# Kernel optimization log

Measured on AMD Instinct MI355X. Metric: run time of the kernel, lower is better.

Reference implementation:

```python
import jax, jax.numpy as jnp
import numpy as np

TEMPERATURE = 2.0


def _offdiag_idx(n):
    # flat indices of the off-diagonal entries of an [n, n] matrix, row-major,
    # reshaped to [n, n-1] (matches torch masked_select(~eye).view(n, n-1))
    idx = np.arange(n * n).reshape(n, n)
    return jnp.asarray(idx[~np.eye(n, dtype=bool)].reshape(n, n - 1))


def setup_inputs() -> dict:
    key = jax.random.key(0)
    k1, k2, k3, k4 = jax.random.split(key, 4)
    B, D = 256, 512
    return {
        "wt_emb": jax.random.normal(k1, (B, D), dtype=jnp.float32),
        "mt_emb": jax.random.normal(k2, (B, D), dtype=jnp.float32),
        "label_wt": jax.random.uniform(k3, (B,), dtype=jnp.float32),
        "label_mt": jax.random.uniform(k4, (B,), dtype=jnp.float32),
    }


def reference(wt_emb, mt_emb, label_wt, label_mt):
    t = TEMPERATURE
    features = jnp.concatenate([wt_emb, mt_emb], axis=0)            # [n, D]
    labels = jnp.concatenate([label_wt, label_mt], axis=0)[:, None]  # [n, 1]
    n = features.shape[0]

    # L1 label differences: [n, n]
    label_diffs = jnp.abs(labels[:, None, :] - labels[None, :, :]).sum(-1)

    # negative L2 feature distances (safe sqrt: diagonal is exactly 0)
    diff = features[:, None, :] - features[None, :, :]               # [n, n, D]
    sq = jnp.sum(diff * diff, axis=-1)                               # [n, n]
    dist = jnp.where(sq > 0, jnp.sqrt(jnp.where(sq > 0, sq, 1.0)), 0.0)
    logits = -dist / t
    logits = logits - jax.lax.stop_gradient(jnp.max(logits, axis=1, keepdims=True))
    exp_logits = jnp.exp(logits)

    # drop diagonal -> [n, n-1]
    off = _offdiag_idx(n)
    lo = logits.reshape(-1)[off]
    eo = exp_logits.reshape(-1)[off]
    ldo = label_diffs.reshape(-1)[off]

    # vectorized over positive index k: mask[i, k, j] = ld[i, j] >= ld[i, k]
    neg_mask = ldo[:, None, :] >= ldo[:, :, None]                    # [n, n-1, n-1]
    denom = jnp.sum(jnp.where(neg_mask, eo[:, None, :], 0.0), axis=-1)  # [n, n-1]
    pos_log_probs = lo - jnp.log(denom)                              # [n, n-1]
    return -jnp.sum(pos_log_probs) / (n * (n - 1))
```

## Files before the change

### kernel.cpp

```cpp
#include <hip/hip_runtime.h>

#define N 512
#define B 256
#define D 512
#define NT 512
#define NBLK (N / 2)

#define WS_SL    0
#define WS_RANK  N
#define WS_NORM  (2 * N)
#define WS_PART  (3 * N)

__global__ __launch_bounds__(NT) void rank_norm_kernel(
    const float* __restrict__ wt, const float* __restrict__ mt,
    const float* __restrict__ lwt, const float* __restrict__ lmt,
    float* __restrict__ ws)
{
    const int t = threadIdx.x, b = blockIdx.x;
    __shared__ float slab[N];
    __shared__ int scnt[32];
    slab[t] = (t < B) ? lwt[t] : lmt[t - B];
    if (t < 32) scnt[t] = 0;
    __syncthreads();

    const int jj = t & 31, j = b * 32 + jj, c = t >> 5;
    const float lj = slab[j];
    int r = 0;
    #pragma unroll 8
    for (int x = c * 32; x < c * 32 + 32; ++x) {
        const float v = slab[x];
        r += (v < lj || (v == lj && x < j)) ? 1 : 0;
    }
    atomicAdd(&scnt[jj], r);

    const int row = b * 32 + (t >> 4), s16 = t & 15;
    const float* F = (row < B) ? (wt + (size_t)row * D) : (mt + (size_t)(row - B) * D);
    const float4* F4 = (const float4*)F;
    float nacc = 0.f;
    #pragma unroll
    for (int q = 0; q < 8; ++q) {
        const float4 v = F4[s16 + 16 * q];
        nacc += v.x * v.x + v.y * v.y + v.z * v.z + v.w * v.w;
    }
    nacc += __shfl_down(nacc, 8, 16);
    nacc += __shfl_down(nacc, 4, 16);
    nacc += __shfl_down(nacc, 2, 16);
    nacc += __shfl_down(nacc, 1, 16);
    if (s16 == 0) ws[WS_NORM + row] = nacc;

    __syncthreads();
    if (t < 32) {
        const int r2 = scnt[t], j2 = b * 32 + t;
        ws[WS_SL + r2] = slab[j2];
        ((int*)ws)[WS_RANK + j2] = r2;
    }
}

__global__ __launch_bounds__(NT) void rnc_main(
    const float* __restrict__ wt, const float* __restrict__ mt,
    const float* __restrict__ lwt, const float* __restrict__ lmt,
    float* __restrict__ ws)
{
    const int b = blockIdx.x, i0 = 2 * b, i1 = 2 * b + 1;
    const int t = threadIdx.x;
    const int w = t >> 6, lane = t & 63, g = lane >> 4, s = lane & 15;

    __shared__ float sl[N];
    __shared__ int   srk[N];
    __shared__ float snm[N];
    __shared__ __align__(16) float sp0[N];
    __shared__ __align__(16) float sf0[N];
    __shared__ __align__(16) float sp1[N];
    __shared__ __align__(16) float sf1[N];
    __shared__ float sred[NT / 64];

    sl[t]  = ws[WS_SL + t];
    srk[t] = ((const int*)ws)[WS_RANK + t];
    snm[t] = ws[WS_NORM + t];

    const float* Fi0 = (i0 < B) ? (wt + (size_t)i0 * D) : (mt + (size_t)(i0 - B) * D);
    const float* Fi1 = (i1 < B) ? (wt + (size_t)i1 * D) : (mt + (size_t)(i1 - B) * D);
    const float4* Fi04 = (const float4*)Fi0;
    const float4* Fi14 = (const float4*)Fi1;
    float4 fr0[8], fr1[8];
    #pragma unroll
    for (int q = 0; q < 8; ++q) { fr0[q] = Fi04[s + 16 * q]; fr1[q] = Fi14[s + 16 * q]; }
    const float li0 = (i0 < B) ? lwt[i0] : lmt[i0 - B];
    const float li1 = (i1 < B) ? lwt[i1] : lmt[i1 - B];
    __syncthreads();
    const float ni0 = snm[i0], ni1 = snm[i1];

    float lg_acc = 0.f;
    const int wg = w * 4 + g;
    for (int m = 0; m < 16; ++m) {
        const int j = wg + 32 * m;
        const float* Fj = (j < B) ? (wt + (size_t)j * D) : (mt + (size_t)(j - B) * D);
        const float4* Fj4 = (const float4*)Fj;
        float a0 = 0.f, a1 = 0.f;
        #pragma unroll
        for (int q = 0; q < 8; ++q) {
            const float4 v = Fj4[s + 16 * q];
            a0 += fr0[q].x * v.x + fr0[q].y * v.y + fr0[q].z * v.z + fr0[q].w * v.w;
            a1 += fr1[q].x * v.x + fr1[q].y * v.y + fr1[q].z * v.z + fr1[q].w * v.w;
        }
        a0 += __shfl_down(a0, 8, 16); a1 += __shfl_down(a1, 8, 16);
        a0 += __shfl_down(a0, 4, 16); a1 += __shfl_down(a1, 4, 16);
        a0 += __shfl_down(a0, 2, 16); a1 += __shfl_down(a1, 2, 16);
        a0 += __shfl_down(a0, 1, 16); a1 += __shfl_down(a1, 1, 16);
        if (s == 0) {
            const float nj = snm[j];
            const float d0 = fmaxf(ni0 + nj - 2.f * a0, 0.f);
            const float d1 = fmaxf(ni1 + nj - 2.f * a1, 0.f);
            const float lg0 = -0.5f * sqrtf(d0);
            const float lg1 = -0.5f * sqrtf(d1);
            lg_acc += lg0 + lg1;
            const int pos = srk[j];
            const float e0 = (j == i0) ? 0.f : __expf(lg0);
            const float e1 = (j == i1) ? 0.f : __expf(lg1);
            sp0[pos] = e0; sf0[pos] = e0;
            sp1[pos] = e1; sf1[pos] = e1;
        }
    }
    __syncthreads();

    if (w < 4) {
        float* arr = (w == 0) ? sp0 : (w == 1) ? sf0 : (w == 2) ? sp1 : sf1;
        float4* a4 = (float4*)arr;
        float4 u0 = a4[lane * 2], u1 = a4[lane * 2 + 1];
        float v0 = u0.x, v1 = u0.y, v2 = u0.z, v3 = u0.w;
        float v4 = u1.x, v5 = u1.y, v6 = u1.z, v7 = u1.w;
        if ((w & 1) == 0) {
            v1 += v0; v2 += v1; v3 += v2; v4 += v3; v5 += v4; v6 += v5; v7 += v6;
            float x = v7;
            #pragma unroll
            for (int off = 1; off < 64; off <<= 1) {
                const float y = __shfl_up(x, off, 64);
                if (lane >= off) x += y;
            }
            float ex = __shfl_up(x, 1, 64);
            if (lane == 0) ex = 0.f;
            v0 += ex; v1 += ex; v2 += ex; v3 += ex; v4 += ex; v5 += ex; v6 += ex; v7 += ex;
        } else {
            v6 += v7; v5 += v6; v4 += v5; v3 += v4; v2 += v3; v1 += v2; v0 += v1;
            float x = v0;
            #pragma unroll
            for (int off = 1; off < 64; off <<= 1) {
                const float y = __shfl_down(x, off, 64);
                if (lane + off < 64) x += y;
            }
            float ex = __shfl_down(x, 1, 64);
            if (lane == 63) ex = 0.f;
            v0 += ex; v1 += ex; v2 += ex; v3 += ex; v4 += ex; v5 += ex; v6 += ex; v7 += ex;
        }
        a4[lane * 2]     = make_float4(v0, v1, v2, v3);
        a4[lane * 2 + 1] = make_float4(v4, v5, v6, v7);
    }
    __syncthreads();

    const int ri0 = srk[i0], ri1 = srk[i1];
    float local = lg_acc;
    #pragma unroll
    for (int p = 0; p < 2; ++p) {
        const int idx = t + p * NT;
        const int row = idx >> 9;
        const int x = idx & (N - 1);
        const int ri = row ? ri1 : ri0;
        const float li = row ? li1 : li0;
        const float* SP = row ? sp1 : sp0;
        const float* SF = row ? sf1 : sf0;
        if (x != ri) {
            const float th = fabsf(li - sl[x]);
            int lo = 0, hi = ri + 1;
            while (lo < hi) {
                const int mid = (lo + hi) >> 1;
                if (fabsf(li - sl[mid]) >= th) lo = mid + 1; else hi = mid;
            }
            const int a = lo;
            lo = ri + 1; hi = N;
            while (lo < hi) {
                const int mid = (lo + hi) >> 1;
                if (fabsf(li - sl[mid]) >= th) hi = mid; else lo = mid + 1;
            }
            const int bb = lo;
            const float denom = ((a > 0) ? SP[a - 1] : 0.f) + ((bb < N) ? SF[bb] : 0.f);
            local -= __logf(denom);
        }
    }

    #pragma unroll
    for (int off = 32; off > 0; off >>= 1)
        local += __shfl_down(local, off, 64);
    if (lane == 0) sred[w] = local;
    __syncthreads();
    if (t == 0) {
        float sum = 0.f;
        #pragma unroll
        for (int k = 0; k < NT / 64; ++k) sum += sred[k];
        ws[WS_PART + b] = sum;
    }
}

__global__ __launch_bounds__(NBLK) void rnc_finalize(
    const float* __restrict__ ws, float* __restrict__ out)
{
    const int t = threadIdx.x;
    __shared__ float sred[NBLK / 64];
    float v = ws[WS_PART + t];
    #pragma unroll
    for (int off = 32; off > 0; off >>= 1)
        v += __shfl_down(v, off, 64);
    if ((t & 63) == 0) sred[t >> 6] = v;
    __syncthreads();
    if (t == 0) {
        float sum = 0.f;
        #pragma unroll
        for (int k = 0; k < NBLK / 64; ++k) sum += sred[k];
        out[0] = -sum / (float)((long)N * (N - 1));
    }
}

extern "C" void kernel_launch(void* const* d_in, const int* in_sizes, int n_in,
                              void* d_out, int out_size, void* d_ws, size_t ws_size,
                              hipStream_t stream) {
    const float* wt  = (const float*)d_in[0];
    const float* mt  = (const float*)d_in[1];
    const float* lwt = (const float*)d_in[2];
    const float* lmt = (const float*)d_in[3];
    float* out = (float*)d_out;
    float* ws  = (float*)d_ws;

    rank_norm_kernel<<<16, NT, 0, stream>>>(wt, mt, lwt, lmt, ws);
    rnc_main<<<NBLK, NT, 0, stream>>>(wt, mt, lwt, lmt, ws);
    rnc_finalize<<<1, NBLK, 0, stream>>>(ws, out);
}
```

Before: 81.37 us.

## Compute row norms inline in main kernel and fuse finalize via atomic last-block reduction

Row squared norms are no longer computed by the rank kernel and staged through workspace. The main kernel now derives them itself: its own two rows from registers, and each column row's norm during the dot-product loop as an extra accumulator. The separate finalize kernel is replaced by an atomic float sum plus a completion counter, and the last block writes the output. This removes one kernel launch and some global round trips, at the cost of extra FMAs and shuffles per column and a nondeterministic atomic summation order.

Result: slower. 92.50 us (+13.7%).

```diff
diff --git a/kernel.cpp b/kernel.cpp
--- a/kernel.cpp
+++ b/kernel.cpp
@@ -8,11 +8,10 @@
 
 #define WS_SL    0
 #define WS_RANK  N
-#define WS_NORM  (2 * N)
-#define WS_PART  (3 * N)
-
-__global__ __launch_bounds__(NT) void rank_norm_kernel(
-    const float* __restrict__ wt, const float* __restrict__ mt,
+#define WS_SUM   (2 * N)
+#define WS_CNT   (2 * N + 1)
+
+__global__ __launch_bounds__(NT) void rank_kernel(
     const float* __restrict__ lwt, const float* __restrict__ lmt,
     float* __restrict__ ws)
 {
@@ -32,34 +31,22 @@
         r += (v < lj || (v == lj && x < j)) ? 1 : 0;
     }
     atomicAdd(&scnt[jj], r);
-
-    const int row = b * 32 + (t >> 4), s16 = t & 15;
-    const float* F = (row < B) ? (wt + (size_t)row * D) : (mt + (size_t)(row - B) * D);
-    const float4* F4 = (const float4*)F;
-    float nacc = 0.f;
-    #pragma unroll
-    for (int q = 0; q < 8; ++q) {
-        const float4 v = F4[s16 + 16 * q];
-        nacc += v.x * v.x + v.y * v.y + v.z * v.z + v.w * v.w;
-    }
-    nacc += __shfl_down(nacc, 8, 16);
-    nacc += __shfl_down(nacc, 4, 16);
-    nacc += __shfl_down(nacc, 2, 16);
-    nacc += __shfl_down(nacc, 1, 16);
-    if (s16 == 0) ws[WS_NORM + row] = nacc;
-
     __syncthreads();
     if (t < 32) {
         const int r2 = scnt[t], j2 = b * 32 + t;
         ws[WS_SL + r2] = slab[j2];
         ((int*)ws)[WS_RANK + j2] = r2;
     }
+    if (b == 0 && t == 0) {
+        ws[WS_SUM] = 0.f;
+        ((unsigned*)ws)[WS_CNT] = 0u;
+    }
 }
 
 __global__ __launch_bounds__(NT) void rnc_main(
     const float* __restrict__ wt, const float* __restrict__ mt,
     const float* __restrict__ lwt, const float* __restrict__ lmt,
-    float* __restrict__ ws)
+    float* __restrict__ ws, float* __restrict__ out)
 {
     const int b = blockIdx.x, i0 = 2 * b, i1 = 2 * b + 1;
     const int t = threadIdx.x;
@@ -67,7 +54,6 @@
 
     __shared__ float sl[N];
     __shared__ int   srk[N];
-    __shared__ float snm[N];
     __shared__ __align__(16) float sp0[N];
     __shared__ __align__(16) float sf0[N];
     __shared__ __align__(16) float sp1[N];
@@ -76,7 +62,6 @@
 
     sl[t]  = ws[WS_SL + t];
     srk[t] = ((const int*)ws)[WS_RANK + t];
-    snm[t] = ws[WS_NORM + t];
 
     const float* Fi0 = (i0 < B) ? (wt + (size_t)i0 * D) : (mt + (size_t)(i0 - B) * D);
     const float* Fi1 = (i1 < B) ? (wt + (size_t)i1 * D) : (mt + (size_t)(i1 - B) * D);
@@ -87,8 +72,20 @@
     for (int q = 0; q < 8; ++q) { fr0[q] = Fi04[s + 16 * q]; fr1[q] = Fi14[s + 16 * q]; }
     const float li0 = (i0 < B) ? lwt[i0] : lmt[i0 - B];
     const float li1 = (i1 < B) ? lwt[i1] : lmt[i1 - B];
-    __syncthreads();
-    const float ni0 = snm[i0], ni1 = snm[i1];
+
+    float ni0 = 0.f, ni1 = 0.f;
+    #pragma unroll
+    for (int q = 0; q < 8; ++q) {
+        ni0 += fr0[q].x * fr0[q].x + fr0[q].y * fr0[q].y
+             + fr0[q].z * fr0[q].z + fr0[q].w * fr0[q].w;
+        ni1 += fr1[q].x * fr1[q].x + fr1[q].y * fr1[q].y
+             + fr1[q].z * fr1[q].z + fr1[q].w * fr1[q].w;
+    }
+    ni0 += __shfl_down(ni0, 8, 16); ni1 += __shfl_down(ni1, 8, 16);
+    ni0 += __shfl_down(ni0, 4, 16); ni1 += __shfl_down(ni1, 4, 16);
+    ni0 += __shfl_down(ni0, 2, 16); ni1 += __shfl_down(ni1, 2, 16);
+    ni0 += __shfl_down(ni0, 1, 16); ni1 += __shfl_down(ni1, 1, 16);
+    __syncthreads();
 
     float lg_acc = 0.f;
     const int wg = w * 4 + g;
@@ -96,21 +93,21 @@
         const int j = wg + 32 * m;
         const float* Fj = (j < B) ? (wt + (size_t)j * D) : (mt + (size_t)(j - B) * D);
         const float4* Fj4 = (const float4*)Fj;
-        float a0 = 0.f, a1 = 0.f;
+        float a0 = 0.f, a1 = 0.f, an = 0.f;
         #pragma unroll
         for (int q = 0; q < 8; ++q) {
             const float4 v = Fj4[s + 16 * q];
             a0 += fr0[q].x * v.x + fr0[q].y * v.y + fr0[q].z * v.z + fr0[q].w * v.w;
             a1 += fr1[q].x * v.x + fr1[q].y * v.y + fr1[q].z * v.z + fr1[q].w * v.w;
-        }
-        a0 += __shfl_down(a0, 8, 16); a1 += __shfl_down(a1, 8, 16);
-        a0 += __shfl_down(a0, 4, 16); a1 += __shfl_down(a1, 4, 16);
-        a0 += __shfl_down(a0, 2, 16); a1 += __shfl_down(a1, 2, 16);
-        a0 += __shfl_down(a0, 1, 16); a1 += __shfl_down(a1, 1, 16);
+            an += v.x * v.x + v.y * v.y + v.z * v.z + v.w * v.w;
+        }
+        a0 += __shfl_down(a0, 8, 16); a1 += __shfl_down(a1, 8, 16); an += __shfl_down(an, 8, 16);
+        a0 += __shfl_down(a0, 4, 16); a1 += __shfl_down(a1, 4, 16); an += __shfl_down(an, 4, 16);
+        a0 += __shfl_down(a0, 2, 16); a1 += __shfl_down(a1, 2, 16); an += __shfl_down(an, 2, 16);
+        a0 += __shfl_down(a0, 1, 16); a1 += __shfl_down(a1, 1, 16); an += __shfl_down(an, 1, 16);
         if (s == 0) {
-            const float nj = snm[j];
-            const float d0 = fmaxf(ni0 + nj - 2.f * a0, 0.f);
-            const float d1 = fmaxf(ni1 + nj - 2.f * a1, 0.f);
+            const float d0 = fmaxf(ni0 + an - 2.f * a0, 0.f);
+            const float d1 = fmaxf(ni1 + an - 2.f * a1, 0.f);
             const float lg0 = -0.5f * sqrtf(d0);
             const float lg1 = -0.5f * sqrtf(d1);
             lg_acc += lg0 + lg1;
@@ -196,26 +193,14 @@
         float sum = 0.f;
         #pragma unroll
         for (int k = 0; k < NT / 64; ++k) sum += sred[k];
-        ws[WS_PART + b] = sum;
-    }
-}
-
-__global__ __launch_bounds__(NBLK) void rnc_finalize(
-    const float* __restrict__ ws, float* __restrict__ out)
-{
-    const int t = threadIdx.x;
-    __shared__ float sred[NBLK / 64];
-    float v = ws[WS_PART + t];
-    #pragma unroll
-    for (int off = 32; off > 0; off >>= 1)
-        v += __shfl_down(v, off, 64);
-    if ((t & 63) == 0) sred[t >> 6] = v;
-    __syncthreads();
-    if (t == 0) {
-        float sum = 0.f;
-        #pragma unroll
-        for (int k = 0; k < NBLK / 64; ++k) sum += sred[k];
-        out[0] = -sum / (float)((long)N * (N - 1));
+        atomicAdd(&ws[WS_SUM], sum);
+        __threadfence();
+        const unsigned old = atomicAdd(&((unsigned*)ws)[WS_CNT], 1u);
+        if (old == NBLK - 1) {
+            __threadfence();
+            const float total = atomicAdd(&ws[WS_SUM], 0.f);
+            out[0] = -total / (float)((long)N * (N - 1));
+        }
     }
 }
 
@@ -229,7 +214,6 @@
     float* out = (float*)d_out;
     float* ws  = (float*)d_ws;
 
-    rank_norm_kernel<<<16, NT, 0, stream>>>(wt, mt, lwt, lmt, ws);
-    rnc_main<<<NBLK, NT, 0, stream>>>(wt, mt, lwt, lmt, ws);
-    rnc_finalize<<<1, NBLK, 0, stream>>>(ws, out);
+    rank_kernel<<<16, NT, 0, stream>>>(lwt, lmt, ws);
+    rnc_main<<<NBLK, NT, 0, stream>>>(wt, mt, lwt, lmt, ws, out);
 }
```

## Permute feature rows into label-sorted order so main kernel indexes directly

Applied to the files above, without the earlier changes.

The first kernel now writes every feature row and its squared norm into a workspace buffer ordered by label rank. The main kernel then reads features from that buffer and indexes rows by rank, so it no longer needs a rank lookup table, per-row wt/mt selection, or global label loads. This adds a 1 MB copy in the prepass to simplify indexing in the main kernel. The change also alters how the diagonal logit is excluded from the accumulated sum.

After: 83.22 us. 2.3% more time.

```diff
diff --git a/kernel.cpp b/kernel.cpp
--- a/kernel.cpp
+++ b/kernel.cpp
@@ -7,11 +7,11 @@
 #define NBLK (N / 2)
 
 #define WS_SL    0
-#define WS_RANK  N
-#define WS_NORM  (2 * N)
-#define WS_PART  (3 * N)
-
-__global__ __launch_bounds__(NT) void rank_norm_kernel(
+#define WS_NORM  512
+#define WS_PART  1024
+#define WS_FS    2048
+
+__global__ __launch_bounds__(NT) void sort_rows_kernel(
     const float* __restrict__ wt, const float* __restrict__ mt,
     const float* __restrict__ lwt, const float* __restrict__ lmt,
     float* __restrict__ ws)
@@ -32,33 +32,32 @@
         r += (v < lj || (v == lj && x < j)) ? 1 : 0;
     }
     atomicAdd(&scnt[jj], r);
+    __syncthreads();
+
+    if (t < 32)
+        ws[WS_SL + scnt[t]] = slab[b * 32 + t];
 
     const int row = b * 32 + (t >> 4), s16 = t & 15;
+    const int rr = scnt[t >> 4];
     const float* F = (row < B) ? (wt + (size_t)row * D) : (mt + (size_t)(row - B) * D);
     const float4* F4 = (const float4*)F;
+    float4* Dst = (float4*)(ws + WS_FS + (size_t)rr * D);
     float nacc = 0.f;
     #pragma unroll
     for (int q = 0; q < 8; ++q) {
-        const float4 v = F4[s16 + 16 * q];
+        const int idx = s16 + 16 * q;
+        const float4 v = F4[idx];
         nacc += v.x * v.x + v.y * v.y + v.z * v.z + v.w * v.w;
+        Dst[idx] = v;
     }
     nacc += __shfl_down(nacc, 8, 16);
     nacc += __shfl_down(nacc, 4, 16);
     nacc += __shfl_down(nacc, 2, 16);
     nacc += __shfl_down(nacc, 1, 16);
-    if (s16 == 0) ws[WS_NORM + row] = nacc;
-
-    __syncthreads();
-    if (t < 32) {
-        const int r2 = scnt[t], j2 = b * 32 + t;
-        ws[WS_SL + r2] = slab[j2];
-        ((int*)ws)[WS_RANK + j2] = r2;
-    }
+    if (s16 == 0) ws[WS_NORM + rr] = nacc;
 }
 
 __global__ __launch_bounds__(NT) void rnc_main(
-    const float* __restrict__ wt, const float* __restrict__ mt,
-    const float* __restrict__ lwt, const float* __restrict__ lmt,
     float* __restrict__ ws)
 {
     const int b = blockIdx.x, i0 = 2 * b, i1 = 2 * b + 1;
@@ -66,7 +65,6 @@
     const int w = t >> 6, lane = t & 63, g = lane >> 4, s = lane & 15;
 
     __shared__ float sl[N];
-    __shared__ int   srk[N];
     __shared__ float snm[N];
     __shared__ __align__(16) float sp0[N];
     __shared__ __align__(16) float sf0[N];
@@ -75,27 +73,23 @@
     __shared__ float sred[NT / 64];
 
     sl[t]  = ws[WS_SL + t];
-    srk[t] = ((const int*)ws)[WS_RANK + t];
     snm[t] = ws[WS_NORM + t];
 
-    const float* Fi0 = (i0 < B) ? (wt + (size_t)i0 * D) : (mt + (size_t)(i0 - B) * D);
-    const float* Fi1 = (i1 < B) ? (wt + (size_t)i1 * D) : (mt + (size_t)(i1 - B) * D);
-    const float4* Fi04 = (const float4*)Fi0;
-    const float4* Fi14 = (const float4*)Fi1;
+    const float* Fs = ws + WS_FS;
+    const float4* Fi04 = (const float4*)(Fs + (size_t)i0 * D);
+    const float4* Fi14 = (const float4*)(Fs + (size_t)i1 * D);
     float4 fr0[8], fr1[8];
     #pragma unroll
     for (int q = 0; q < 8; ++q) { fr0[q] = Fi04[s + 16 * q]; fr1[q] = Fi14[s + 16 * q]; }
-    const float li0 = (i0 < B) ? lwt[i0] : lmt[i0 - B];
-    const float li1 = (i1 < B) ? lwt[i1] : lmt[i1 - B];
-    __syncthreads();
+    __syncthreads();
+    const float li0 = sl[i0], li1 = sl[i1];
     const float ni0 = snm[i0], ni1 = snm[i1];
 
     float lg_acc = 0.f;
     const int wg = w * 4 + g;
     for (int m = 0; m < 16; ++m) {
         const int j = wg + 32 * m;
-        const float* Fj = (j < B) ? (wt + (size_t)j * D) : (mt + (size_t)(j - B) * D);
-        const float4* Fj4 = (const float4*)Fj;
+        const float4* Fj4 = (const float4*)(Fs + (size_t)j * D);
         float a0 = 0.f, a1 = 0.f;
         #pragma unroll
         for (int q = 0; q < 8; ++q) {
@@ -113,12 +107,12 @@
             const float d1 = fmaxf(ni1 + nj - 2.f * a1, 0.f);
             const float lg0 = -0.5f * sqrtf(d0);
             const float lg1 = -0.5f * sqrtf(d1);
-            lg_acc += lg0 + lg1;
-            const int pos = srk[j];
+            if (j != i0) lg_acc += lg0;
+            if (j != i1) lg_acc += lg1;
             const float e0 = (j == i0) ? 0.f : __expf(lg0);
             const float e1 = (j == i1) ? 0.f : __expf(lg1);
-            sp0[pos] = e0; sf0[pos] = e0;
-            sp1[pos] = e1; sf1[pos] = e1;
+            sp0[j] = e0; sf0[j] = e0;
+            sp1[j] = e1; sf1[j] = e1;
         }
     }
     __syncthreads();
@@ -157,14 +151,13 @@
     }
     __syncthreads();
 
-    const int ri0 = srk[i0], ri1 = srk[i1];
     float local = lg_acc;
     #pragma unroll
     for (int p = 0; p < 2; ++p) {
         const int idx = t + p * NT;
         const int row = idx >> 9;
         const int x = idx & (N - 1);
-        const int ri = row ? ri1 : ri0;
+        const int ri = row ? i1 : i0;
         const float li = row ? li1 : li0;
         const float* SP = row ? sp1 : sp0;
         const float* SF = row ? sf1 : sf0;
@@ -229,7 +222,7 @@
     float* out = (float*)d_out;
     float* ws  = (float*)d_ws;
 
-    rank_norm_kernel<<<16, NT, 0, stream>>>(wt, mt, lwt, lmt, ws);
-    rnc_main<<<NBLK, NT, 0, stream>>>(wt, mt, lwt, lmt, ws);
+    sort_rows_kernel<<<16, NT, 0, stream>>>(wt, mt, lwt, lmt, ws);
+    rnc_main<<<NBLK, NT, 0, stream>>>(ws);
     rnc_finalize<<<1, NBLK, 0, stream>>>(ws, out);
 }
```
